# Kernel tuning notes

Hardware: AMD Instinct MI355X
Metric: run time of the kernel (lower is better)

The kernel has to match this reference:

```python
import jax, jax.numpy as jnp
import numpy as np

RECALL_THRESHOLD = 0.3
LAMBDA_PAUC = 0.5
NUM_CLASSES = 128
LABEL_SMOOTHING = 0.1
N_SAMPLES = 131072


def setup_inputs() -> dict:
    key = jax.random.key(0)
    k1, k2 = jax.random.split(key)
    predictions = jax.random.normal(k1, (N_SAMPLES, NUM_CLASSES), dtype=jnp.float32)
    targets = jax.random.randint(k2, (N_SAMPLES,), 0, NUM_CLASSES)
    return {"predictions": predictions, "targets": targets}


def _macro_pauc(probs, targets):
    """Vectorized (over classes) partial AUC at max_fpr = 1 - recall_threshold.

    Equivalent to the per-class torch loop: descending argsort of scores,
    cumsum TP/FP, clip the ROC curve at max_fpr with linear interpolation of
    the crossing segment, trapezoidal integration, macro-average over classes
    that have at least one positive.
    """
    N, K = probs.shape
    order = jnp.argsort(-probs, axis=0)                      # [N, K] descending per class
    t_sorted = (targets[order] == jnp.arange(K)[None, :]).astype(probs.dtype)  # [N, K]
    tps = jnp.cumsum(t_sorted, axis=0)                        # [N, K]
    fps = jnp.cumsum(1.0 - t_sorted, axis=0)                  # [N, K]
    tpr = tps / jnp.maximum(tps[-1], 1.0)
    fpr = fps / jnp.maximum(fps[-1], 1.0)

    max_fpr = 1.0 - RECALL_THRESHOLD
    # Clip fpr at max_fpr; segments fully beyond the cut get delta == 0 so
    # their tpr value is irrelevant. The crossing segment's right endpoint is
    # replaced by the linearly interpolated tpr at max_fpr (matches torch's
    # slope-based interpolation with the same 1e-8 guard).
    fpr_c = jnp.minimum(fpr, max_fpr)
    slope = (tpr[1:] - tpr[:-1]) / (fpr[1:] - fpr[:-1] + 1e-8)
    tpr_interp = tpr[:-1] + slope * (max_fpr - fpr[:-1])
    tpr_next = jnp.where(fpr[1:] <= max_fpr, tpr[1:], tpr_interp)
    delta = fpr_c[1:] - fpr_c[:-1]                            # [N-1, K]
    pauc_c = jnp.sum(delta * 0.5 * (tpr_next + tpr[:-1]), axis=0)  # [K]

    valid = (tps[-1] > 0).astype(probs.dtype)                 # macro: skip empty classes
    return jnp.sum(pauc_c * valid) / jnp.maximum(jnp.sum(valid), 1.0)


def reference(predictions, targets):
    logp = jax.nn.log_softmax(predictions, axis=1)
    probs = jnp.exp(logp)
    # CrossEntropyLoss with label smoothing (mean reduction, no class weights):
    # loss_i = (1-eps) * nll_i + eps * mean_c(-log p_ic)
    nll = -jnp.take_along_axis(logp, targets[:, None], axis=1)[:, 0]
    smooth = -jnp.mean(logp, axis=1)
    ce_loss = jnp.mean((1.0 - LABEL_SMOOTHING) * nll + LABEL_SMOOTHING * smooth)

    # torch.tensor(pauc) in the original detaches pAUC from the graph.
    pauc = jax.lax.stop_gradient(_macro_pauc(probs, targets))
    pauc_loss = 1.0 - pauc ** 2
    return (1.0 - LAMBDA_PAUC) * ce_loss + LAMBDA_PAUC * pauc_loss
```

## Files before the change

### kernel.cpp

```cpp
#include <hip/hip_runtime.h>
#include <math.h>

#define N_SAMPLES 131072
#define NUM_CLASSES 128
#define NB 64
#define MAX_FPR 0.7f
#define NBLK 512
#define ROWS_PER_BLK 256
#define HP 33
#define PART_WORDS (NUM_CLASSES * 32 * 2)

typedef unsigned int u32;

__device__ __forceinline__ int bin_of(float x, float off ) {
    int b = (int)__fmaf_rn(x, 4.0f, off);
    return min(max(b, 0), NB - 1);
}

__global__ __launch_bounds__(1024, 8) void fused_kernel(
    const float* __restrict__ pred, const int* __restrict__ tgt,
    u32* __restrict__ part,
    float* __restrict__ ceArr,
    u32* __restrict__ doneCtr)
{
    __shared__ u32 hA[NUM_CLASSES * HP];
    __shared__ u32 hP[NUM_CLASSES * HP];
    __shared__ float wsum[16];

    const int tid  = threadIdx.x;
    const int w    = tid >> 6;
    const int lane = tid & 63;
    const int j    = lane & 15;
    const int rs   = lane >> 4;

    for (int i = tid; i < NUM_CLASSES * HP; i += 1024) { hA[i] = 0u; hP[i] = 0u; }
    if (blockIdx.x == 0 && tid == 0) *doneCtr = 0u;
    __syncthreads();

    const int rowBase = blockIdx.x * ROWS_PER_BLK + w * 4 + rs;
    float acc_lse = 0.0f, acc_xt = 0.0f, acc_sx = 0.0f;

    const float* r0p = pred + (size_t)rowBase * 128;
    float4 a0 = *(const float4*)(r0p + j * 4);
    float4 a1 = *(const float4*)(r0p + 64 + j * 4);
    int    ta = tgt[rowBase];
    const float* r1p = r0p + (size_t)64 * 128;
    float4 c0 = *(const float4*)(r1p + j * 4);
    float4 c1 = *(const float4*)(r1p + 64 + j * 4);
    int    tb = tgt[rowBase + 64];

    #pragma unroll
    for (int p = 0; p < 4; p++) {
        float4 n0, n1; int tn = 0;
        if (p < 2) {
            const float* rn = pred + (size_t)(rowBase + (p + 2) * 64) * 128;
            n0 = *(const float4*)(rn + j * 4);
            n1 = *(const float4*)(rn + 64 + j * 4);
            tn = tgt[rowBase + (p + 2) * 64];
        }

        float e = __expf(a0.x) + __expf(a0.y) + __expf(a0.z) + __expf(a0.w)
                + __expf(a1.x) + __expf(a1.y) + __expf(a1.z) + __expf(a1.w);
        #pragma unroll
        for (int o = 1; o < 16; o <<= 1) e += __shfl_xor(e, o);
        const float lse = __logf(e);
        const float off = (14.0f - lse) * 4.0f;

        const float xv[8] = {a0.x, a0.y, a0.z, a0.w, a1.x, a1.y, a1.z, a1.w};
        #pragma unroll
        for (int q = 0; q < 8; q++) {
            const int c = (q < 4) ? (j * 4 + q) : (64 + j * 4 + (q - 4));
            const int b = bin_of(xv[q], off);
            const int word = ((b >> 1) + j) & 31;
            atomicAdd(&hA[c * HP + word], (b & 1) ? 65536u : 1u);
        }

        acc_sx  += (xv[0] + xv[1] + xv[2] + xv[3])
                 + (xv[4] + xv[5] + xv[6] + xv[7]);
        acc_lse += lse * 0.0625f;

        {
            const int t = ta;
            float xt; bool hit = false;
            if ((t >> 2) == j)                        { xt = xv[t & 3];       hit = true; }
            else if (t >= 64 && ((t - 64) >> 2) == j) { xt = xv[4 + (t & 3)]; hit = true; }
            if (hit) {
                acc_xt += xt;
                const int bp = bin_of(xt, off);
                atomicAdd(&hP[t * HP + (((bp >> 1) + j) & 31)],
                          (bp & 1) ? 65536u : 1u);
            }
        }

        a0 = c0; a1 = c1; ta = tb;
        c0 = n0; c1 = n1; tb = tn;
    }

    float ce = acc_lse - 0.9f * acc_xt - (0.1f / 128.0f) * acc_sx;
    #pragma unroll
    for (int o = 32; o; o >>= 1) ce += __shfl_xor(ce, o);
    if (lane == 0) wsum[w] = ce;
    __syncthreads();
    if (tid == 0) {
        float s = 0.0f;
        #pragma unroll
        for (int i = 0; i < 16; i++) s += wsum[i];
        ceArr[blockIdx.x] = s;
    }

    u32* outp = part + (size_t)blockIdx.x * PART_WORDS;
    for (int i = tid; i < 4096; i += 1024) {
        const int c = i >> 5, bw = i & 31;
        const int src = c * HP + ((bw + ((c >> 2) & 15)) & 31);
        outp[i]        = hA[src];
        outp[4096 + i] = hP[src];
    }
}

__global__ __launch_bounds__(256) void pauc_reduce(
    const u32* __restrict__ part, const float* __restrict__ ceArr,
    float* __restrict__ paucArr, float* __restrict__ validArr,
    u32* __restrict__ doneCtr, float* __restrict__ out)
{
    __shared__ u32 aB[NB], pB[NB];

    const int k  = blockIdx.x;
    const int t  = threadIdx.x;
    const int w  = t & 31;
    const int sl = t >> 5;

    if (t < NB) { aB[t] = 0u; pB[t] = 0u; }
    __syncthreads();

    u32 alo = 0u, ahi = 0u, plo = 0u, phi = 0u;
    const u32* base = part + (size_t)(sl * 64) * PART_WORDS + k * 32 + w;
    #pragma unroll 8
    for (int b = 0; b < 64; b++) {
        const u32 qa = base[(size_t)b * PART_WORDS];
        const u32 qp = base[(size_t)b * PART_WORDS + 4096];
        alo += qa & 0xffffu; ahi += qa >> 16;
        plo += qp & 0xffffu; phi += qp >> 16;
    }
    atomicAdd(&aB[2 * w], alo); atomicAdd(&aB[2 * w + 1], ahi);
    atomicAdd(&pB[2 * w], plo); atomicAdd(&pB[2 * w + 1], phi);
    __syncthreads();

    if (t < 64) {
        const int l = t;
        const u32 a = aB[63 - l];
        const u32 p = pB[63 - l];

        u32 ia = a, ip = p;
        #pragma unroll
        for (int o = 1; o < 64; o <<= 1) {
            const u32 tA = __shfl_up(ia, o);
            const u32 tP = __shfl_up(ip, o);
            if (l >= o) { ia += tA; ip += tP; }
        }
        const u32 P = __shfl(ip, 63);
        const u32 T = __shfl(ia, 63);
        const float Pm = fmaxf((float)P, 1.0f);
        const float Fm = fmaxf((float)(T - P), 1.0f);

        const int cumA = (int)(ia - a), cumP = (int)(ip - p);
        float contrib = 0.0f;
        const int f = (int)a - (int)p;
        if (f > 0) {
            const float fpr0 = (float)(cumA - cumP) / Fm;
            if (fpr0 < MAX_FPR) {
                const float tpr0 = (float)cumP / Pm;
                const float tpr1 = (float)(cumP + (int)p) / Pm;
                const float fpr1 = (float)(cumA - cumP + f) / Fm;
                if (fpr1 <= MAX_FPR) {
                    contrib = (fpr1 - fpr0) * 0.5f * (tpr0 + tpr1);
                } else {
                    const float tfrac = (MAX_FPR - fpr0) / (fpr1 - fpr0);
                    const float tprc  = tpr0 + tfrac * (tpr1 - tpr0);
                    contrib = (MAX_FPR - fpr0) * 0.5f * (tpr0 + tprc);
                }
            }
        }
        #pragma unroll
        for (int o = 32; o; o >>= 1) contrib += __shfl_xor(contrib, o);

        int isLast = 0;
        if (l == 0) {
            paucArr[k]  = (P > 0u) ? contrib : 0.0f;
            validArr[k] = (P > 0u) ? 1.0f : 0.0f;
            __threadfence();
            const u32 tk = atomicAdd(doneCtr, 1u);
            isLast = (tk == NUM_CLASSES - 1);
        }
        isLast = __shfl(isLast, 0);

        if (isLast) {
            float s1 = 0.0f, s2 = 0.0f, s3 = 0.0f;
            #pragma unroll
            for (int i = l; i < NUM_CLASSES; i += 64) {
                s1 += __hip_atomic_load(paucArr + i,  __ATOMIC_RELAXED,
                                        __HIP_MEMORY_SCOPE_AGENT);
                s2 += __hip_atomic_load(validArr + i, __ATOMIC_RELAXED,
                                        __HIP_MEMORY_SCOPE_AGENT);
            }
            #pragma unroll
            for (int i = l; i < NBLK; i += 64) s3 += ceArr[i];
            #pragma unroll
            for (int o = 32; o; o >>= 1) {
                s1 += __shfl_xor(s1, o);
                s2 += __shfl_xor(s2, o);
                s3 += __shfl_xor(s3, o);
            }
            if (l == 0) {
                const float cem  = s3 * (1.0f / (float)N_SAMPLES);
                const float pauc = s1 / fmaxf(s2, 1.0f);
                out[0] = 0.5f * cem + 0.5f * (1.0f - pauc * pauc);
            }
        }
    }
}

extern "C" void kernel_launch(void* const* d_in, const int* in_sizes, int n_in,
                              void* d_out, int out_size, void* d_ws, size_t ws_size,
                              hipStream_t stream)
{
    const float* pred = (const float*)d_in[0];
    const int*   tgt  = (const int*)d_in[1];

    char* ws = (char*)d_ws;
    u32*   part    = (u32*)ws;
    float* ceArr   = (float*)(ws + 16777216);
    float* paucArr = (float*)(ws + 16777216 + 2048);
    float* validArr= (float*)(ws + 16777216 + 2560);
    u32*   doneCtr = (u32*)  (ws + 16777216 + 3072);

    fused_kernel<<<NBLK, 1024, 0, stream>>>(pred, tgt, part, ceArr, doneCtr);
    pauc_reduce<<<NUM_CLASSES, 256, 0, stream>>>(part, ceArr, paucArr, validArr,
                                                 doneCtr, (float*)d_out);
}
```

Baseline: 104.8 us.

## Fuse pAUC reduction into main kernel via global atomics and last-block finish

Instead of writing per-block histogram partials (16 MB) and running a second reduction kernel, each block atomically adds its nonzero histogram bins into a small global histogram. The last block to finish, chosen by an atomic ticket, computes the per-class ROC integration and the final loss. A memset now clears the global bins and counter before launch. This removes the large partial-buffer traffic and one kernel launch, at the cost of many global atomics contending on 16K counters and a serialized tail done by a single block.

```diff
diff --git a/kernel.cpp b/kernel.cpp
--- a/kernel.cpp
+++ b/kernel.cpp
@@ -8,7 +8,6 @@
 #define NBLK 512
 #define ROWS_PER_BLK 256
 #define HP 33
-#define PART_WORDS (NUM_CLASSES * 32 * 2)
 
 typedef unsigned int u32;
 
@@ -19,13 +18,18 @@
 
 __global__ __launch_bounds__(1024, 8) void fused_kernel(
     const float* __restrict__ pred, const int* __restrict__ tgt,
-    u32* __restrict__ part,
+    u32* __restrict__ gAll,
+    u32* __restrict__ gPos,
+    u32* __restrict__ doneCtr,
     float* __restrict__ ceArr,
-    u32* __restrict__ doneCtr)
+    float* __restrict__ out)
 {
     __shared__ u32 hA[NUM_CLASSES * HP];
     __shared__ u32 hP[NUM_CLASSES * HP];
     __shared__ float wsum[16];
+    __shared__ float pauc_s[NUM_CLASSES];
+    __shared__ float valid_s[NUM_CLASSES];
+    __shared__ u32 tkt;
 
     const int tid  = threadIdx.x;
     const int w    = tid >> 6;
@@ -34,7 +38,6 @@
     const int rs   = lane >> 4;
 
     for (int i = tid; i < NUM_CLASSES * HP; i += 1024) { hA[i] = 0u; hP[i] = 0u; }
-    if (blockIdx.x == 0 && tid == 0) *doneCtr = 0u;
     __syncthreads();
 
     const int rowBase = blockIdx.x * ROWS_PER_BLK + w * 4 + rs;
@@ -108,47 +111,29 @@
         ceArr[blockIdx.x] = s;
     }
 
-    u32* outp = part + (size_t)blockIdx.x * PART_WORDS;
-    for (int i = tid; i < 4096; i += 1024) {
-        const int c = i >> 5, bw = i & 31;
-        const int src = c * HP + ((bw + ((c >> 2) & 15)) & 31);
-        outp[i]        = hA[src];
-        outp[4096 + i] = hP[src];
-    }
-}
-
-__global__ __launch_bounds__(256) void pauc_reduce(
-    const u32* __restrict__ part, const float* __restrict__ ceArr,
-    float* __restrict__ paucArr, float* __restrict__ validArr,
-    u32* __restrict__ doneCtr, float* __restrict__ out)
-{
-    __shared__ u32 aB[NB], pB[NB];
-
-    const int k  = blockIdx.x;
-    const int t  = threadIdx.x;
-    const int w  = t & 31;
-    const int sl = t >> 5;
-
-    if (t < NB) { aB[t] = 0u; pB[t] = 0u; }
-    __syncthreads();
-
-    u32 alo = 0u, ahi = 0u, plo = 0u, phi = 0u;
-    const u32* base = part + (size_t)(sl * 64) * PART_WORDS + k * 32 + w;
-    #pragma unroll 8
-    for (int b = 0; b < 64; b++) {
-        const u32 qa = base[(size_t)b * PART_WORDS];
-        const u32 qp = base[(size_t)b * PART_WORDS + 4096];
-        alo += qa & 0xffffu; ahi += qa >> 16;
-        plo += qp & 0xffffu; phi += qp >> 16;
-    }
-    atomicAdd(&aB[2 * w], alo); atomicAdd(&aB[2 * w + 1], ahi);
-    atomicAdd(&pB[2 * w], plo); atomicAdd(&pB[2 * w + 1], phi);
-    __syncthreads();
-
-    if (t < 64) {
-        const int l = t;
-        const u32 a = aB[63 - l];
-        const u32 p = pB[63 - l];
+    for (int i = tid; i < NUM_CLASSES * NB; i += 1024) {
+        const int c  = i >> 6, b = i & 63;
+        const int sw = c * HP + (((b >> 1) + ((c >> 2) & 15)) & 31);
+        const u32 wa = hA[sw];
+        const u32 wp = hP[sw];
+        const u32 ca = (b & 1) ? (wa >> 16) : (wa & 0xffffu);
+        const u32 cp = (b & 1) ? (wp >> 16) : (wp & 0xffffu);
+        if (ca) atomicAdd(&gAll[i], ca);
+        if (cp) atomicAdd(&gPos[i], cp);
+    }
+
+    __syncthreads();
+    if (tid == 0) { __threadfence(); tkt = atomicAdd(doneCtr, 1u); }
+    __syncthreads();
+    if (tkt != NBLK - 1u) return;
+
+    for (int r = 0; r < 8; r++) {
+        const int k = w * 8 + r;
+        const int l = lane;
+        const u32 a = __hip_atomic_load(&gAll[k * 64 + 63 - l],
+                                        __ATOMIC_RELAXED, __HIP_MEMORY_SCOPE_AGENT);
+        const u32 p = __hip_atomic_load(&gPos[k * 64 + 63 - l],
+                                        __ATOMIC_RELAXED, __HIP_MEMORY_SCOPE_AGENT);
 
         u32 ia = a, ip = p;
         #pragma unroll
@@ -182,39 +167,31 @@
         }
         #pragma unroll
         for (int o = 32; o; o >>= 1) contrib += __shfl_xor(contrib, o);
-
-        int isLast = 0;
         if (l == 0) {
-            paucArr[k]  = (P > 0u) ? contrib : 0.0f;
-            validArr[k] = (P > 0u) ? 1.0f : 0.0f;
-            __threadfence();
-            const u32 tk = atomicAdd(doneCtr, 1u);
-            isLast = (tk == NUM_CLASSES - 1);
-        }
-        isLast = __shfl(isLast, 0);
-
-        if (isLast) {
-            float s1 = 0.0f, s2 = 0.0f, s3 = 0.0f;
-            #pragma unroll
-            for (int i = l; i < NUM_CLASSES; i += 64) {
-                s1 += __hip_atomic_load(paucArr + i,  __ATOMIC_RELAXED,
-                                        __HIP_MEMORY_SCOPE_AGENT);
-                s2 += __hip_atomic_load(validArr + i, __ATOMIC_RELAXED,
-                                        __HIP_MEMORY_SCOPE_AGENT);
-            }
-            #pragma unroll
-            for (int i = l; i < NBLK; i += 64) s3 += ceArr[i];
-            #pragma unroll
-            for (int o = 32; o; o >>= 1) {
-                s1 += __shfl_xor(s1, o);
-                s2 += __shfl_xor(s2, o);
-                s3 += __shfl_xor(s3, o);
-            }
-            if (l == 0) {
-                const float cem  = s3 * (1.0f / (float)N_SAMPLES);
-                const float pauc = s1 / fmaxf(s2, 1.0f);
-                out[0] = 0.5f * cem + 0.5f * (1.0f - pauc * pauc);
-            }
+            pauc_s[k]  = (P > 0u) ? contrib : 0.0f;
+            valid_s[k] = (P > 0u) ? 1.0f : 0.0f;
+        }
+    }
+    __syncthreads();
+
+    if (w == 0) {
+        float s1 = pauc_s[lane] + pauc_s[lane + 64];
+        float s2 = valid_s[lane] + valid_s[lane + 64];
+        float s3 = 0.0f;
+        #pragma unroll
+        for (int i = 0; i < 8; i++)
+            s3 += __hip_atomic_load(ceArr + lane + i * 64,
+                                    __ATOMIC_RELAXED, __HIP_MEMORY_SCOPE_AGENT);
+        #pragma unroll
+        for (int o = 32; o; o >>= 1) {
+            s1 += __shfl_xor(s1, o);
+            s2 += __shfl_xor(s2, o);
+            s3 += __shfl_xor(s3, o);
+        }
+        if (lane == 0) {
+            const float cem  = s3 * (1.0f / (float)N_SAMPLES);
+            const float pauc = s1 / fmaxf(s2, 1.0f);
+            out[0] = 0.5f * cem + 0.5f * (1.0f - pauc * pauc);
         }
     }
 }
@@ -227,13 +204,12 @@
     const int*   tgt  = (const int*)d_in[1];
 
     char* ws = (char*)d_ws;
-    u32*   part    = (u32*)ws;
-    float* ceArr   = (float*)(ws + 16777216);
-    float* paucArr = (float*)(ws + 16777216 + 2048);
-    float* validArr= (float*)(ws + 16777216 + 2560);
-    u32*   doneCtr = (u32*)  (ws + 16777216 + 3072);
-
-    fused_kernel<<<NBLK, 1024, 0, stream>>>(pred, tgt, part, ceArr, doneCtr);
-    pauc_reduce<<<NUM_CLASSES, 256, 0, stream>>>(part, ceArr, paucArr, validArr,
-                                                 doneCtr, (float*)d_out);
+    u32*   gAll    = (u32*)ws;
+    u32*   gPos    = (u32*)(ws + 32768);
+    u32*   doneCtr = (u32*)(ws + 65536);
+    float* ceArr   = (float*)(ws + 66560);
+
+    hipMemsetAsync(ws, 0, 66560, stream);
+    fused_kernel<<<NBLK, 1024, 0, stream>>>(pred, tgt, gAll, gPos, doneCtr,
+                                            ceArr, (float*)d_out);
 }
```

Result: slower. 119.6 us (+14.2%).
